# Kernel optimization log

Hardware: AMD Instinct MI355X
Metric: run time of the kernel (lower is better)

Reference implementation:

```python
import jax, jax.numpy as jnp
import numpy as np

D_MODEL = 256
NUM_HEADS = 8
DIM_HEAD = D_MODEL // NUM_HEADS
EPS = 1e-6
MASK_BIAS = -1.0e9


def setup_inputs() -> dict:
    key = jax.random.key(0)
    ks = jax.random.split(key, 10)
    B, S = 2, 4096
    x = jax.random.normal(ks[0], (B, S, D_MODEL), dtype=jnp.float32)
    pad_mask = jnp.zeros((B, S), dtype=jnp.float32)  # 1.0 => padded position
    scale = 1.0 / np.sqrt(D_MODEL)
    Wq = jax.random.normal(ks[1], (D_MODEL, D_MODEL), dtype=jnp.float32) * scale
    bq = jnp.zeros((D_MODEL,), dtype=jnp.float32)
    Wk = jax.random.normal(ks[2], (D_MODEL, D_MODEL), dtype=jnp.float32) * scale
    bk = jnp.zeros((D_MODEL,), dtype=jnp.float32)
    Wv = jax.random.normal(ks[3], (D_MODEL, D_MODEL), dtype=jnp.float32) * scale
    bv = jnp.zeros((D_MODEL,), dtype=jnp.float32)
    gamma = jnp.ones((D_MODEL,), dtype=jnp.float32)
    beta = jnp.zeros((D_MODEL,), dtype=jnp.float32)
    return {"x": x, "pad_mask": pad_mask, "Wq": Wq, "bq": bq, "Wk": Wk,
            "bk": bk, "Wv": Wv, "bv": bv, "gamma": gamma, "beta": beta}


def _layer_norm(h, gamma, beta):
    mu = jnp.mean(h, axis=-1, keepdims=True)
    var = jnp.mean(jnp.square(h - mu), axis=-1, keepdims=True)
    return gamma * (h - mu) * jax.lax.rsqrt(var + EPS) + beta


def reference(x, pad_mask, Wq, bq, Wk, bk, Wv, bv, gamma, beta):
    B, S, D = x.shape
    q = x @ Wq + bq  # [B,S,D]
    k = x @ Wk + bk
    v = x @ Wv + bv
    # split heads: [B,S,D] -> [B,H,S,Dh]
    def split(t):
        return t.reshape(B, S, NUM_HEADS, DIM_HEAD).transpose(0, 2, 1, 3)
    qh, kh, vh = split(q), split(k), split(v)
    w = jnp.einsum("bhqd,bhkd->bhqk", qh, kh)  # [B,H,S,S]
    # faithful to source: mask added BEFORE the 1/sqrt(dim_head) scaling
    w = w + pad_mask[:, None, None, :] * MASK_BIAS
    w = w / jnp.sqrt(jnp.float32(DIM_HEAD))
    attn = jax.nn.softmax(w, axis=-1)
    # dropout is identity at inference
    out = jnp.einsum("bhqk,bhkd->bhqd", attn, vh)  # [B,H,S,Dh]
    out = out.transpose(0, 2, 1, 3).reshape(B, S, D)
    return _layer_norm(out + x, gamma, beta)
```

## Files before the change

### kernel.cpp

```cpp
#include <hip/hip_runtime.h>
#include <hip/hip_bf16.h>

#define D_MODEL 256
#define NUM_HEADS 8
#define DIM_HEAD 32
#define SEQ 4096
#define BATCH 2
#define NROWS (BATCH * SEQ)
#define LN_EPS 1e-6f
#define MASK_BIAS -1.0e9f
#define SCALE 0.17677669529663687f
#define LOG2E 1.4426950408889634f
#define QSCALE (SCALE * LOG2E)

typedef __attribute__((ext_vector_type(8))) short short8;
typedef __attribute__((ext_vector_type(4))) float f32x4;

static __device__ __forceinline__ unsigned short f2b(float f) {
    union { __hip_bfloat16 b; unsigned short u; } cv;
    cv.b = __float2bfloat16(f);
    return cv.u;
}
static __device__ __forceinline__ unsigned int pk_bf16(float lo, float hi) {
    union { __hip_bfloat162 v; unsigned int u; } cv;
    cv.v = __float22bfloat162_rn(make_float2(lo, hi));
    return cv.u;
}
static __device__ __forceinline__ float exp2_raw(float x) {
#if __has_builtin(__builtin_amdgcn_exp2f)
    return __builtin_amdgcn_exp2f(x);
#else
    float r;
    asm volatile("v_exp_f32 %0, %1" : "=v"(r) : "v"(x));
    return r;
#endif
}
static __device__ __forceinline__ void load_lds16(const void* g, void* l) {
    __builtin_amdgcn_global_load_lds(
        (const __attribute__((address_space(1))) unsigned int*)g,
        (__attribute__((address_space(3))) unsigned int*)l, 16, 0, 0);
}

__global__ __launch_bounds__(256) void prep_kernel(
    const float* __restrict__ Wq, const float* __restrict__ Wk,
    const float* __restrict__ Wv,
    const float* __restrict__ bq, const float* __restrict__ bk,
    const float* __restrict__ bv,
    const float* __restrict__ pad,
    unsigned short* __restrict__ Wt, float* __restrict__ biasc,
    float* __restrict__ T2)
{
    const int blk = blockIdx.x;
    const int t = threadIdx.x;
    if (blk < 768) {
        const int w = blk >> 8;
        const int k = blk & 255;
        const float* W = (w == 0) ? Wq : (w == 1) ? Wk : Wv;
        Wt[(size_t)(w * 256 + t) * 256 + k] = f2b(W[(size_t)k * 256 + t]);
        if (k == 0) {
            const float* bb = (w == 0) ? bq : (w == 1) ? bk : bv;
            biasc[w * 256 + t] = bb[t];
        }
    } else {
        const int i = (blk - 768) * 256 + t;
        T2[i] = pad[i] * (MASK_BIAS * SCALE * LOG2E);
    }
}

__global__ __launch_bounds__(256) void qkv_mfma_kernel(
    const float* __restrict__ x, const unsigned short* __restrict__ Wt,
    const float* __restrict__ biasc,
    unsigned short* __restrict__ Qh, unsigned short* __restrict__ Kh,
    unsigned short* __restrict__ Vt)
{
    const int lane = threadIdx.x & 63;
    const int wid  = threadIdx.x >> 6;
    const int c    = lane & 15;
    const int quad = lane >> 4;

    const int r0 = (blockIdx.x >> 3) * 64 + wid * 16;
    const int n0 = (blockIdx.x & 7) * 96;

    f32x4 acc[6];
    float bias[6];
    #pragma unroll
    for (int t = 0; t < 6; t++) {
        acc[t] = (f32x4){0.f, 0.f, 0.f, 0.f};
        bias[t] = biasc[n0 + 16 * t + c];
    }

    const float* xp0 = x + (size_t)(r0 + c) * D_MODEL + quad * 8;
    const unsigned short* wp0 = Wt + (size_t)(n0 + c) * 256 + quad * 8;

    for (int k0 = 0; k0 < 256; k0 += 32) {
        const float4 a0 = *(const float4*)(xp0 + k0);
        const float4 a1 = *(const float4*)(xp0 + k0 + 4);
        union { unsigned int u[4]; short8 s; } af;
        af.u[0] = pk_bf16(a0.x, a0.y);
        af.u[1] = pk_bf16(a0.z, a0.w);
        af.u[2] = pk_bf16(a1.x, a1.y);
        af.u[3] = pk_bf16(a1.z, a1.w);
        #pragma unroll
        for (int t = 0; t < 6; t++) {
            const short8 bf = *(const short8*)(wp0 + (size_t)(16 * t) * 256 + k0);
            acc[t] = __builtin_amdgcn_mfma_f32_16x16x32_bf16(af.s, bf, acc[t], 0, 0, 0);
        }
    }

    #pragma unroll
    for (int t = 0; t < 6; t++) {
        const int col = n0 + 16 * t;
        const int mm  = col >> 8;
        const int dim = (col & 255) + c;
        const int h = dim >> 5, d = dim & 31;
        const int row = r0 + quad * 4;
        const int bb = row >> 12;
        const int s  = row & (SEQ - 1);
        const size_t bh = (size_t)(bb * NUM_HEADS + h);
        float v0 = acc[t][0] + bias[t];
        float v1 = acc[t][1] + bias[t];
        float v2 = acc[t][2] + bias[t];
        float v3 = acc[t][3] + bias[t];
        if (mm == 2) {
            uint2 pk = make_uint2(pk_bf16(v0, v1), pk_bf16(v2, v3));
            *(uint2*)(Vt + (bh * DIM_HEAD + d) * SEQ + s) = pk;
        } else {
            if (mm == 0) {
                v0 *= QSCALE; v1 *= QSCALE; v2 *= QSCALE; v3 *= QSCALE;
            }
            unsigned short* P = (mm == 0 ? Qh : Kh) + (bh * SEQ + s) * DIM_HEAD + d;
            P[0]  = f2b(v0);
            P[32] = f2b(v1);
            P[64] = f2b(v2);
            P[96] = f2b(v3);
        }
    }
}

__global__ __launch_bounds__(256, 4) void attn_mfma_kernel(
    const unsigned short* __restrict__ Qh, const unsigned short* __restrict__ Kh,
    const unsigned short* __restrict__ Vt, const float* __restrict__ T2,
    float* __restrict__ O)
{
    __shared__ __align__(16) unsigned short ldsK[3][64 * 32];
    __shared__ __align__(16) unsigned short ldsV[3][32 * 64];
    __shared__ __align__(16) float          ldsT[3][64];

    const int lane = threadIdx.x & 63;
    const int wid  = threadIdx.x >> 6;
    const int c    = lane & 15;
    const int quad = lane >> 4;

    const int gw = blockIdx.x;
    const int q0 = (gw & 63) * 64;
    const int h  = (gw >> 6) & (NUM_HEADS - 1);
    const int b  = gw >> 9;
    const size_t bh = (size_t)(b * NUM_HEADS + h);

    const int perm = ((c & 12) << 1) | (c & 3);

    const unsigned short* Kb = Kh + bh * SEQ * DIM_HEAD;
    const unsigned short* Vb = Vt + bh * DIM_HEAD * SEQ;
    const float* Tb = T2 + (size_t)b * SEQ;

    const int qrow = q0 + wid * 16;
    const short8 qf = *(const short8*)(Qh + (bh * SEQ + qrow + c) * DIM_HEAD + quad * 8);

    union { unsigned int u[4]; short8 s; } ones;
    ones.u[0] = ones.u[1] = ones.u[2] = ones.u[3] = 0x3F803F80u;

    const int f0 = ((perm >> 1) ^ (perm >> 3)) & 3;
    const int f1 = (((perm + 4) >> 1) ^ ((perm + 4) >> 3)) & 3;
    const int kA = perm * 32 + ((quad ^ f0) << 3);
    const int kB = (perm + 4) * 32 + ((quad ^ f1) << 3);
    const int g0 = quad ^ (c & 7);
    const int vA0 = c * 64 + (g0 << 3);
    const int vA1 = c * 64 + ((g0 ^ 4) << 3);
    const int vB0 = (16 + c) * 64 + (g0 << 3);
    const int vB1 = (16 + c) * 64 + ((g0 ^ 4) << 3);

    const int skey = (lane >> 2);
    const int sgK  = lane & 3;
    const int sdim = lane >> 3;
    const int sgV  = lane & 7;

    f32x4 o0 = {0.f,0.f,0.f,0.f}, o1 = {0.f,0.f,0.f,0.f};
    f32x4 lacc = {0.f,0.f,0.f,0.f};

    auto stage = [&](int ch, int pb) {
        const int s0 = ch * 64;
        if (wid < 2) {
            #pragma unroll
            for (int jj = 0; jj < 2; jj++) {
                const int j = wid * 2 + jj;
                const int key = j * 16 + skey;
                const int f = ((key >> 1) ^ (key >> 3)) & 3;
                load_lds16(Kb + (size_t)(s0 + key) * 32 + ((sgK ^ f) << 3),
                           &ldsK[pb][j * 512]);
            }
        } else {
            #pragma unroll
            for (int jj = 0; jj < 2; jj++) {
                const int j = (wid - 2) * 2 + jj;
                const int dim = j * 8 + sdim;
                load_lds16(Vb + (size_t)dim * SEQ + s0 + ((sgV ^ (dim & 7)) << 3),
                           &ldsV[pb][j * 512]);
            }
            if (wid == 3 && lane < 16)
                load_lds16(Tb + s0 + lane * 4, &ldsT[pb][0]);
        }
    };

    auto sub = [&](int pb, int s) {
        const short8 kf0 = *(const short8*)&ldsK[pb][s * 1024 + kA];
        const short8 kf1 = *(const short8*)&ldsK[pb][s * 1024 + kB];
        const short8 vf0 = *(const short8*)&ldsV[pb][s ? vA1 : vA0];
        const short8 vf1 = *(const short8*)&ldsV[pb][s ? vB1 : vB0];
        const float4 t0 = *(const float4*)&ldsT[pb][s * 32 + quad * 8];
        const float4 t1 = *(const float4*)&ldsT[pb][s * 32 + quad * 8 + 4];

        const f32x4 c0 = {t0.x, t0.y, t0.z, t0.w};
        const f32x4 c1 = {t1.x, t1.y, t1.z, t1.w};
        const f32x4 st0 = __builtin_amdgcn_mfma_f32_16x16x32_bf16(kf0, qf, c0, 0, 0, 0);
        const f32x4 st1 = __builtin_amdgcn_mfma_f32_16x16x32_bf16(kf1, qf, c1, 0, 0, 0);

        float p[8];
        p[0] = exp2_raw(st0[0]);
        p[1] = exp2_raw(st0[1]);
        p[2] = exp2_raw(st0[2]);
        p[3] = exp2_raw(st0[3]);
        p[4] = exp2_raw(st1[0]);
        p[5] = exp2_raw(st1[1]);
        p[6] = exp2_raw(st1[2]);
        p[7] = exp2_raw(st1[3]);

        union { unsigned int u[4]; short8 s8; } pf;
        pf.u[0] = pk_bf16(p[0], p[1]);
        pf.u[1] = pk_bf16(p[2], p[3]);
        pf.u[2] = pk_bf16(p[4], p[5]);
        pf.u[3] = pk_bf16(p[6], p[7]);

        lacc = __builtin_amdgcn_mfma_f32_16x16x32_bf16(ones.s, pf.s8, lacc, 0, 0, 0);
        o0   = __builtin_amdgcn_mfma_f32_16x16x32_bf16(vf0,   pf.s8, o0,   0, 0, 0);
        o1   = __builtin_amdgcn_mfma_f32_16x16x32_bf16(vf1,   pf.s8, o1,   0, 0, 0);
    };

    stage(0, 0);
    stage(1, 1);

    int rb = 0;
    int sb = 2;
    for (int ch = 0; ch < SEQ / 64; ++ch) {
        if (wid == 3)
            asm volatile("s_waitcnt vmcnt(3) lgkmcnt(0)" ::: "memory");
        else
            asm volatile("s_waitcnt vmcnt(2) lgkmcnt(0)" ::: "memory");
        __builtin_amdgcn_s_barrier();
        __builtin_amdgcn_sched_barrier(0);
        stage((ch + 2) & 63, sb);
        sub(rb, 0);
        sub(rb, 1);
        rb = (rb == 2) ? 0 : rb + 1;
        sb = (sb == 2) ? 0 : sb + 1;
    }

    const float inv = 1.0f / lacc[0];
    float* op = O + ((size_t)(b * SEQ) + qrow + c) * D_MODEL + h * DIM_HEAD + quad * 4;
    *(float4*)op        = make_float4(o0[0]*inv, o0[1]*inv, o0[2]*inv, o0[3]*inv);
    *(float4*)(op + 16) = make_float4(o1[0]*inv, o1[1]*inv, o1[2]*inv, o1[3]*inv);
}

__global__ __launch_bounds__(256) void ln_kernel(
    float* AO,
    const float* __restrict__ x,
    const float* __restrict__ gamma, const float* __restrict__ beta)
{
    const int lane = threadIdx.x & 63;
    const int wid  = threadIdx.x >> 6;
    const size_t row = (size_t)blockIdx.x * 4 + wid;

    const float4 a  = ((const float4*)(AO + row * D_MODEL))[lane];
    const float4 xv = ((const float4*)(x + row * D_MODEL))[lane];
    float hv[4];
    hv[0] = a.x + xv.x;
    hv[1] = a.y + xv.y;
    hv[2] = a.z + xv.z;
    hv[3] = a.w + xv.w;

    float s = hv[0] + hv[1] + hv[2] + hv[3];
    #pragma unroll
    for (int off = 32; off > 0; off >>= 1) s += __shfl_xor(s, off, 64);
    const float mu = s * (1.0f / D_MODEL);

    float d0 = hv[0]-mu, d1 = hv[1]-mu, d2 = hv[2]-mu, d3 = hv[3]-mu;
    float ss = d0*d0 + d1*d1 + d2*d2 + d3*d3;
    #pragma unroll
    for (int off = 32; off > 0; off >>= 1) ss += __shfl_xor(ss, off, 64);
    const float rs = rsqrtf(ss * (1.0f / D_MODEL) + LN_EPS);

    const float4 g  = ((const float4*)gamma)[lane];
    const float4 bb = ((const float4*)beta)[lane];
    float4 y;
    y.x = g.x * d0 * rs + bb.x;
    y.y = g.y * d1 * rs + bb.y;
    y.z = g.z * d2 * rs + bb.z;
    y.w = g.w * d3 * rs + bb.w;
    ((float4*)(AO + row * D_MODEL))[lane] = y;
}

extern "C" void kernel_launch(void* const* d_in, const int* in_sizes, int n_in,
                              void* d_out, int out_size, void* d_ws, size_t ws_size,
                              hipStream_t stream)
{
    const float* x     = (const float*)d_in[0];
    const float* pad   = (const float*)d_in[1];
    const float* Wq    = (const float*)d_in[2];
    const float* bq    = (const float*)d_in[3];
    const float* Wk    = (const float*)d_in[4];
    const float* bk    = (const float*)d_in[5];
    const float* Wv    = (const float*)d_in[6];
    const float* bv    = (const float*)d_in[7];
    const float* gamma = (const float*)d_in[8];
    const float* beta  = (const float*)d_in[9];

    const size_t elems = (size_t)NROWS * D_MODEL;
    unsigned short* Qh = (unsigned short*)d_ws;
    unsigned short* Kh = Qh + elems;
    unsigned short* Vt = Kh + elems;
    float* T2 = (float*)(Vt + elems);
    unsigned short* Wt = (unsigned short*)(T2 + NROWS);
    float* biasc = (float*)(Wt + 768 * 256);
    float* AO = (float*)d_out;

    prep_kernel<<<800, 256, 0, stream>>>(Wq, Wk, Wv, bq, bk, bv, pad,
                                         Wt, biasc, T2);
    qkv_mfma_kernel<<<(NROWS / 64) * 8, 256, 0, stream>>>(x, Wt, biasc,
                                                          Qh, Kh, Vt);
    attn_mfma_kernel<<<BATCH * NUM_HEADS * (SEQ / 64), 256, 0, stream>>>(
        Qh, Kh, Vt, T2, AO);
    ln_kernel<<<NROWS / 4, 256, 0, stream>>>(AO, x, gamma, beta);
}
```

Measured before the change: 178.5 us.

## Process two 16-row query tiles per wave in attention kernel

Each wave now handles 32 query rows instead of 16, so each block covers 128 queries and the grid is halved. Every K/V tile staged into LDS and read into registers is reused across two query tiles, which halves global and LDS traffic per unit of work and gives the scheduler more independent MFMAs to interleave. The cost is more accumulator registers, which is why launch bounds drop to 2 blocks per CU, and fewer blocks (512) to fill the GPU.

Measured after the change: 178.2 us. No clear change (-0.2%).

```diff
diff --git a/kernel.cpp b/kernel.cpp
--- a/kernel.cpp
+++ b/kernel.cpp
@@ -137,7 +137,7 @@
     }
 }
 
-__global__ __launch_bounds__(256, 4) void attn_mfma_kernel(
+__global__ __launch_bounds__(256, 2) void attn_mfma_kernel(
     const unsigned short* __restrict__ Qh, const unsigned short* __restrict__ Kh,
     const unsigned short* __restrict__ Vt, const float* __restrict__ T2,
     float* __restrict__ O)
@@ -152,9 +152,9 @@
     const int quad = lane >> 4;
 
     const int gw = blockIdx.x;
-    const int q0 = (gw & 63) * 64;
-    const int h  = (gw >> 6) & (NUM_HEADS - 1);
-    const int b  = gw >> 9;
+    const int q0 = (gw & 31) * 128;
+    const int h  = (gw >> 5) & (NUM_HEADS - 1);
+    const int b  = gw >> 8;
     const size_t bh = (size_t)(b * NUM_HEADS + h);
 
     const int perm = ((c & 12) << 1) | (c & 3);
@@ -163,8 +163,9 @@
     const unsigned short* Vb = Vt + bh * DIM_HEAD * SEQ;
     const float* Tb = T2 + (size_t)b * SEQ;
 
-    const int qrow = q0 + wid * 16;
-    const short8 qf = *(const short8*)(Qh + (bh * SEQ + qrow + c) * DIM_HEAD + quad * 8);
+    const int qrow = q0 + wid * 32;
+    const short8 qfA = *(const short8*)(Qh + (bh * SEQ + qrow + c) * DIM_HEAD + quad * 8);
+    const short8 qfB = *(const short8*)(Qh + (bh * SEQ + qrow + 16 + c) * DIM_HEAD + quad * 8);
 
     union { unsigned int u[4]; short8 s; } ones;
     ones.u[0] = ones.u[1] = ones.u[2] = ones.u[3] = 0x3F803F80u;
@@ -184,8 +185,9 @@
     const int sdim = lane >> 3;
     const int sgV  = lane & 7;
 
-    f32x4 o0 = {0.f,0.f,0.f,0.f}, o1 = {0.f,0.f,0.f,0.f};
-    f32x4 lacc = {0.f,0.f,0.f,0.f};
+    f32x4 oA0 = {0.f,0.f,0.f,0.f}, oA1 = {0.f,0.f,0.f,0.f};
+    f32x4 oB0 = {0.f,0.f,0.f,0.f}, oB1 = {0.f,0.f,0.f,0.f};
+    f32x4 laccA = {0.f,0.f,0.f,0.f}, laccB = {0.f,0.f,0.f,0.f};
 
     auto stage = [&](int ch, int pb) {
         const int s0 = ch * 64;
@@ -221,28 +223,40 @@
 
         const f32x4 c0 = {t0.x, t0.y, t0.z, t0.w};
         const f32x4 c1 = {t1.x, t1.y, t1.z, t1.w};
-        const f32x4 st0 = __builtin_amdgcn_mfma_f32_16x16x32_bf16(kf0, qf, c0, 0, 0, 0);
-        const f32x4 st1 = __builtin_amdgcn_mfma_f32_16x16x32_bf16(kf1, qf, c1, 0, 0, 0);
-
-        float p[8];
-        p[0] = exp2_raw(st0[0]);
-        p[1] = exp2_raw(st0[1]);
-        p[2] = exp2_raw(st0[2]);
-        p[3] = exp2_raw(st0[3]);
-        p[4] = exp2_raw(st1[0]);
-        p[5] = exp2_raw(st1[1]);
-        p[6] = exp2_raw(st1[2]);
-        p[7] = exp2_raw(st1[3]);
-
-        union { unsigned int u[4]; short8 s8; } pf;
-        pf.u[0] = pk_bf16(p[0], p[1]);
-        pf.u[1] = pk_bf16(p[2], p[3]);
-        pf.u[2] = pk_bf16(p[4], p[5]);
-        pf.u[3] = pk_bf16(p[6], p[7]);
-
-        lacc = __builtin_amdgcn_mfma_f32_16x16x32_bf16(ones.s, pf.s8, lacc, 0, 0, 0);
-        o0   = __builtin_amdgcn_mfma_f32_16x16x32_bf16(vf0,   pf.s8, o0,   0, 0, 0);
-        o1   = __builtin_amdgcn_mfma_f32_16x16x32_bf16(vf1,   pf.s8, o1,   0, 0, 0);
+
+        const f32x4 sA0 = __builtin_amdgcn_mfma_f32_16x16x32_bf16(kf0, qfA, c0, 0, 0, 0);
+        const f32x4 sA1 = __builtin_amdgcn_mfma_f32_16x16x32_bf16(kf1, qfA, c1, 0, 0, 0);
+        const f32x4 sB0 = __builtin_amdgcn_mfma_f32_16x16x32_bf16(kf0, qfB, c0, 0, 0, 0);
+        const f32x4 sB1 = __builtin_amdgcn_mfma_f32_16x16x32_bf16(kf1, qfB, c1, 0, 0, 0);
+
+        union { unsigned int u[4]; short8 s8; } pfA, pfB;
+        {
+            float p0 = exp2_raw(sA0[0]), p1 = exp2_raw(sA0[1]);
+            float p2 = exp2_raw(sA0[2]), p3 = exp2_raw(sA0[3]);
+            float p4 = exp2_raw(sA1[0]), p5 = exp2_raw(sA1[1]);
+            float p6 = exp2_raw(sA1[2]), p7 = exp2_raw(sA1[3]);
+            pfA.u[0] = pk_bf16(p0, p1);
+            pfA.u[1] = pk_bf16(p2, p3);
+            pfA.u[2] = pk_bf16(p4, p5);
+            pfA.u[3] = pk_bf16(p6, p7);
+        }
+        {
+            float p0 = exp2_raw(sB0[0]), p1 = exp2_raw(sB0[1]);
+            float p2 = exp2_raw(sB0[2]), p3 = exp2_raw(sB0[3]);
+            float p4 = exp2_raw(sB1[0]), p5 = exp2_raw(sB1[1]);
+            float p6 = exp2_raw(sB1[2]), p7 = exp2_raw(sB1[3]);
+            pfB.u[0] = pk_bf16(p0, p1);
+            pfB.u[1] = pk_bf16(p2, p3);
+            pfB.u[2] = pk_bf16(p4, p5);
+            pfB.u[3] = pk_bf16(p6, p7);
+        }
+
+        laccA = __builtin_amdgcn_mfma_f32_16x16x32_bf16(ones.s, pfA.s8, laccA, 0, 0, 0);
+        laccB = __builtin_amdgcn_mfma_f32_16x16x32_bf16(ones.s, pfB.s8, laccB, 0, 0, 0);
+        oA0   = __builtin_amdgcn_mfma_f32_16x16x32_bf16(vf0,   pfA.s8, oA0,   0, 0, 0);
+        oA1   = __builtin_amdgcn_mfma_f32_16x16x32_bf16(vf1,   pfA.s8, oA1,   0, 0, 0);
+        oB0   = __builtin_amdgcn_mfma_f32_16x16x32_bf16(vf0,   pfB.s8, oB0,   0, 0, 0);
+        oB1   = __builtin_amdgcn_mfma_f32_16x16x32_bf16(vf1,   pfB.s8, oB1,   0, 0, 0);
     };
 
     stage(0, 0);
@@ -264,10 +278,14 @@
         sb = (sb == 2) ? 0 : sb + 1;
     }
 
-    const float inv = 1.0f / lacc[0];
-    float* op = O + ((size_t)(b * SEQ) + qrow + c) * D_MODEL + h * DIM_HEAD + quad * 4;
-    *(float4*)op        = make_float4(o0[0]*inv, o0[1]*inv, o0[2]*inv, o0[3]*inv);
-    *(float4*)(op + 16) = make_float4(o1[0]*inv, o1[1]*inv, o1[2]*inv, o1[3]*inv);
+    const float invA = 1.0f / laccA[0];
+    const float invB = 1.0f / laccB[0];
+    float* opA = O + ((size_t)(b * SEQ) + qrow + c) * D_MODEL + h * DIM_HEAD + quad * 4;
+    float* opB = O + ((size_t)(b * SEQ) + qrow + 16 + c) * D_MODEL + h * DIM_HEAD + quad * 4;
+    *(float4*)opA        = make_float4(oA0[0]*invA, oA0[1]*invA, oA0[2]*invA, oA0[3]*invA);
+    *(float4*)(opA + 16) = make_float4(oA1[0]*invA, oA1[1]*invA, oA1[2]*invA, oA1[3]*invA);
+    *(float4*)opB        = make_float4(oB0[0]*invB, oB0[1]*invB, oB0[2]*invB, oB0[3]*invB);
+    *(float4*)(opB + 16) = make_float4(oB1[0]*invB, oB1[1]*invB, oB1[2]*invB, oB1[3]*invB);
 }
 
 __global__ __launch_bounds__(256) void ln_kernel(
@@ -336,7 +354,7 @@
                                          Wt, biasc, T2);
     qkv_mfma_kernel<<<(NROWS / 64) * 8, 256, 0, stream>>>(x, Wt, biasc,
                                                           Qh, Kh, Vt);
-    attn_mfma_kernel<<<BATCH * NUM_HEADS * (SEQ / 64), 256, 0, stream>>>(
+    attn_mfma_kernel<<<BATCH * NUM_HEADS * (SEQ / 128), 256, 0, stream>>>(
         Qh, Kh, Vt, T2, AO);
     ln_kernel<<<NROWS / 4, 256, 0, stream>>>(AO, x, gamma, beta);
 }
```
